# Performance work log

Measured on AMD Instinct MI355X. Metric: run time of the kernel, lower is better.

Reference implementation:

```python
import jax, jax.numpy as jnp
import numpy as np

IMAGE_SIZE = 224
EPS = 1e-8


def _minmax_global(x, eps=EPS):
    # torch normalize_minmax: global min-max over the whole tensor,
    # returning zeros if the range is degenerate.
    lo = x.min()
    hi = x.max()
    y = (x - lo) / (hi - lo + eps)
    return jnp.where(hi - lo < eps, jnp.zeros_like(x), y)


def setup_inputs() -> dict:
    key = jax.random.key(0)
    x = jax.random.normal(key, (16, 1024, 8), dtype=jnp.float32)  # [B, L, D]
    return {"x": x}


def reference(x):
    B, L, D = x.shape
    # --- gramian_angular_field ---
    x_norm = _minmax_global(x) * 2.0 - 1.0                      # [B, L, D]
    theta = jnp.arccos(jnp.clip(x_norm, -1.0 + 1e-6, 1.0 - 1e-6))
    th = jnp.transpose(theta, (0, 2, 1))                        # [B, D, L]
    # fused batched pairwise cos-sum (replaces B*D python-loop kernels)
    cos_sum = jnp.cos(th[:, :, :, None] + th[:, :, None, :])    # [B, D, L, L]
    # per-(b,d) min-max normalization in one pass
    lo = cos_sum.min(axis=(2, 3), keepdims=True)
    hi = cos_sum.max(axis=(2, 3), keepdims=True)
    gaf = jnp.where(hi - lo < EPS,
                    jnp.zeros_like(cos_sum),
                    (cos_sum - lo) / (hi - lo + EPS))
    gaf = gaf.mean(axis=1, keepdims=True)                       # [B, 1, L, L]
    # bilinear resize, align_corners=False (half-pixel centers)
    gaf = jax.image.resize(gaf, (B, 1, IMAGE_SIZE, IMAGE_SIZE),
                           method="linear", antialias=False)
    gaf = jnp.repeat(gaf, 3, axis=1)                            # RGB (grayscale=False)
    # --- final norm(): global shift/scale ---
    out = gaf - gaf.min()
    out = out / (out.max() + 1e-6)
    return out
```

## Files before the change

kernel.cpp:

```cpp
#include <hip/hip_runtime.h>
#include <math.h>

#define B_ 16
#define L_ 1024
#define IMG 224
#define PIX (IMG*IMG)
#define NBD 128

#define OFF_A     0
#define OFF_TERM  128
#define OFF_GPMIN 256
#define OFF_GPMAX 768
#define OFF_T     1280
#define OFF_G     58624

#define CPAD(k) ((((k) >> 4) * 17) + ((k) & 15))

__device__ __forceinline__ float cclip(float xn) {
    return fminf(fmaxf(xn, -1.0f + 1e-6f), 1.0f - 1e-6f);
}
__device__ __forceinline__ int bucketf(float c) {
    int k = (int)((c + 1.0f) * 512.0f);
    return min(1023, max(0, k));
}

template <int NTHR>
__device__ __forceinline__ void block_minmax_share(float mn, float mx, float* red) {
    #pragma unroll
    for (int off = 32; off > 0; off >>= 1) {
        mn = fminf(mn, __shfl_down(mn, off));
        mx = fmaxf(mx, __shfl_down(mx, off));
    }
    const int lane = threadIdx.x & 63;
    const int wave = threadIdx.x >> 6;
    if (lane == 0) { red[2 + wave*2] = mn; red[3 + wave*2] = mx; }
    __syncthreads();
    if (threadIdx.x == 0) {
        #pragma unroll
        for (int w = 1; w < NTHR/64; ++w) {
            mn = fminf(mn, red[2 + w*2]);
            mx = fmaxf(mx, red[3 + w*2]);
        }
        red[0] = mn; red[1] = mx;
    }
    __syncthreads();
}

__global__ __launch_bounds__(1024) void k_bd(const float* __restrict__ x,
                                             float* __restrict__ wsf) {
    __shared__ float red[36];
    __shared__ float corig[L_];
    __shared__ float arr[L_];
    __shared__ int   cnt[1090];
    __shared__ int   pref[1090];
    const int bd = blockIdx.x;
    const int b = bd >> 3, d = bd & 7;
    const int t = threadIdx.x;

    {
        float mn = 1e30f, mx = -1e30f;
        const float4* xv = (const float4*)x;
        #pragma unroll 4
        for (int i = t; i < 32768; i += 1024) {
            float4 v = xv[i];
            mn = fminf(mn, fminf(fminf(v.x, v.y), fminf(v.z, v.w)));
            mx = fmaxf(mx, fmaxf(fmaxf(v.x, v.y), fmaxf(v.z, v.w)));
        }
        block_minmax_share<1024>(mn, mx, red);
    }
    float lo = red[0], hi = red[1], r = hi - lo, sc, sh;
    if (r < 1e-8f) { sc = 0.0f; sh = -1.0f; }
    else           { sc = 2.0f / (r + 1e-8f); sh = -lo*sc - 1.0f; }

    cnt[t] = 0;
    if (t < 66) cnt[1024 + t] = 0;
    float c = cclip(x[((size_t)(b*L_ + t))*8 + d]*sc + sh);
    corig[t] = c;
    block_minmax_share<1024>(c, c, red);
    float cMin = red[0], cMax = red[1];

    atomicAdd(&cnt[CPAD(bucketf(c))], 1);
    __syncthreads();

    if (t < 64) {
        int s = 0;
        #pragma unroll
        for (int e = 0; e < 16; ++e) s += cnt[t*17 + e];
        int v = s;
        #pragma unroll
        for (int o = 1; o < 64; o <<= 1) {
            int u = __shfl_up(v, o);
            if (t >= o) v += u;
        }
        int run = v - s;
        #pragma unroll
        for (int e = 0; e < 16; ++e) { pref[t*17 + e] = run; run += cnt[t*17 + e]; }
        if (t == 63) pref[CPAD(1024)] = run;
    }
    __syncthreads();
    cnt[CPAD(t)] = pref[CPAD(t)];
    __syncthreads();
    {
        int p = atomicAdd(&cnt[CPAD(bucketf(c))], 1);
        arr[p] = c;
    }
    __syncthreads();

    float rowmin = 1e30f;
    {
        float ci = c;
        float si = sqrtf(fmaxf(1.0f - ci*ci, 0.0f));
        int kt = bucketf(-ci);
        int lo_p = pref[CPAD(kt)], hi_p = pref[CPAD(kt + 1)];
        int start = lo_p, end = hi_p;
        if (lo_p > 0)   start = pref[CPAD(bucketf(arr[lo_p - 1]))];
        if (hi_p < L_)  end   = pref[CPAD(bucketf(arr[hi_p]) + 1)];
        for (int p = start; p < end; ++p) {
            float cj = arr[p];
            float sj = sqrtf(fmaxf(1.0f - cj*cj, 0.0f));
            rowmin = fminf(rowmin, ci*cj - si*sj);
        }
    }
    block_minmax_share<1024>(rowmin, -1e30f, red);
    if (t == 0) {
        float plo = red[0];
        float phi = fmaxf(2.0f*cMin*cMin - 1.0f, 2.0f*cMax*cMax - 1.0f);
        float rr  = phi - plo;
        float inv = (rr < 1e-8f) ? 0.0f : 1.0f / (rr + 1e-8f);
        wsf[OFF_A + bd]    = inv * 0.125f;
        wsf[OFF_TERM + bd] = plo * inv * 0.125f;
    }

    if (t < IMG) {
        const float SC = 1024.0f / 224.0f;
        float syf = (t + 0.5f)*SC - 0.5f;
        int i0 = (int)floorf(syf);
        i0 = max(0, min(i0, L_ - 2));
        float f = syf - (float)i0;
        float ca = corig[i0], cb = corig[i0 + 1];
        float sa = sqrtf(fmaxf(1.0f - ca*ca, 0.0f));
        float sb = sqrtf(fmaxf(1.0f - cb*cb, 0.0f));
        size_t base = OFF_T + ((size_t)(b*IMG + t))*16;
        wsf[base + d]     = ca + f*(cb - ca);
        wsf[base + 8 + d] = sa + f*(sb - sa);
    }
}

__global__ __launch_bounds__(256) void k_resize(float* __restrict__ wsf) {
    __shared__ float lds_y[112];
    __shared__ float red[16];
    int b     = blockIdx.x >> 5;
    int strip = blockIdx.x & 31;
    const float* tb = wsf + OFF_T + (size_t)b*IMG*16;
    int t = threadIdx.x;
    if (t < 112) lds_y[t] = tb[strip*112 + t];
    __syncthreads();
    int ox = min(t, IMG-1);
    bool active = (t < IMG);
    const float4* xt = (const float4*)(tb + (size_t)ox*16);
    float4 cx0 = xt[0], cx1 = xt[1], sx0 = xt[2], sx1 = xt[3];
    const float4* av = (const float4*)(wsf + OFF_A + b*8);
    float4 a0 = av[0], a1 = av[1];
    float bias = 0.f;
    #pragma unroll
    for (int dd = 0; dd < 8; ++dd) bias += wsf[OFF_TERM + b*8 + dd];
    float mn = 1e30f, mx = -1e30f;
    #pragma unroll
    for (int rr = 0; rr < 7; ++rr) {
        const float* Y = lds_y + rr*16;
        float acc;
        acc  = (a0.x*Y[0])*cx0.x - (a0.x*Y[ 8])*sx0.x;
        acc += (a0.y*Y[1])*cx0.y - (a0.y*Y[ 9])*sx0.y;
        acc += (a0.z*Y[2])*cx0.z - (a0.z*Y[10])*sx0.z;
        acc += (a0.w*Y[3])*cx0.w - (a0.w*Y[11])*sx0.w;
        acc += (a1.x*Y[4])*cx1.x - (a1.x*Y[12])*sx1.x;
        acc += (a1.y*Y[5])*cx1.y - (a1.y*Y[13])*sx1.y;
        acc += (a1.z*Y[6])*cx1.z - (a1.z*Y[14])*sx1.z;
        acc += (a1.w*Y[7])*cx1.w - (a1.w*Y[15])*sx1.w;
        float g = acc - bias;
        if (active) {
            int oy = strip*7 + rr;
            wsf[OFF_G + ((size_t)(b*IMG + oy))*IMG + ox] = g;
            mn = fminf(mn, g);
            mx = fmaxf(mx, g);
        }
    }
    block_minmax_share<256>(mn, mx, red);
    if (t == 0) {
        wsf[OFF_GPMIN + blockIdx.x] = red[0];
        wsf[OFF_GPMAX + blockIdx.x] = red[1];
    }
}

__global__ __launch_bounds__(256) void k_out(const float* __restrict__ wsf,
                                             float* __restrict__ out) {
    __shared__ float red[16];
    int t = threadIdx.x;
    float pmn = fminf(wsf[OFF_GPMIN + t], wsf[OFF_GPMIN + t + 256]);
    float pmx = fmaxf(wsf[OFF_GPMAX + t], wsf[OFF_GPMAX + t + 256]);
    block_minmax_share<256>(pmn, pmx, red);
    float gmin = red[0];
    float scale = 1.0f / ((red[1] - gmin) + 1e-6f);
    int idx = blockIdx.x*256 + t;
    float4 gv = ((const float4*)(wsf + OFF_G))[idx];
    float4 v;
    v.x = (gv.x - gmin)*scale;
    v.y = (gv.y - gmin)*scale;
    v.z = (gv.z - gmin)*scale;
    v.w = (gv.w - gmin)*scale;
    int b   = idx / (PIX/4);
    int rem = idx - b*(PIX/4);
    float4* ob = (float4*)(out + (size_t)b*3*PIX) + rem;
    ob[0]         = v;
    ob[PIX/4]     = v;
    ob[2*(PIX/4)] = v;
}

extern "C" void kernel_launch(void* const* d_in, const int* in_sizes, int n_in,
                              void* d_out, int out_size, void* d_ws, size_t ws_size,
                              hipStream_t stream) {
    const float* x = (const float*)d_in[0];
    float* out     = (float*)d_out;
    float* wsf     = (float*)d_ws;

    k_bd    <<<NBD,            1024, 0, stream>>>(x, wsf);
    k_resize<<<512,            256,  0, stream>>>(wsf);
    k_out   <<<(B_*PIX/4)/256, 256,  0, stream>>>(wsf, out);
}
```

Before: 28.07 us.

## Fuse resize into k_bd using inter-block flag barrier per batch

Removes the separate resize kernel launch by having the 8 blocks of each batch signal one another through global flag words and spin-wait until all per-d coefficients are written. Each block then computes 28 output rows of the resized image, reusing its pooled LDS, and writes the per-block min/max partials. This saves one kernel launch and its tail, but it relies on all 128 blocks being co-resident and adds spin-wait latency. Only 128 blocks now do the resize work instead of 512.

```diff
diff --git a/kernel.cpp b/kernel.cpp
--- a/kernel.cpp
+++ b/kernel.cpp
@@ -6,13 +6,15 @@
 #define IMG 224
 #define PIX (IMG*IMG)
 #define NBD 128
-
-#define OFF_A     0
-#define OFF_TERM  128
-#define OFF_GPMIN 256
-#define OFF_GPMAX 768
-#define OFF_T     1280
-#define OFF_G     58624
+#define MAGIC 0x1357BEEFu
+
+#define OFF_DONE  0
+#define OFF_A     1024
+#define OFF_TERM  1152
+#define OFF_GPMIN 1280
+#define OFF_GPMAX 1408
+#define OFF_T     1536
+#define OFF_G     58880
 
 #define CPAD(k) ((((k) >> 4) * 17) + ((k) & 15))
 
@@ -47,12 +49,16 @@
 }
 
 __global__ __launch_bounds__(1024) void k_bd(const float* __restrict__ x,
-                                             float* __restrict__ wsf) {
+                                             float* __restrict__ wsf,
+                                             unsigned* __restrict__ wsu) {
     __shared__ float red[36];
-    __shared__ float corig[L_];
-    __shared__ float arr[L_];
-    __shared__ int   cnt[1090];
-    __shared__ int   pref[1090];
+    __shared__ __align__(16) float POOL[4352];
+    float* corig = POOL;
+    float* arr   = POOL + 1024;
+    int*   cnt   = (int*)(POOL + 2048);
+    int*   pref  = ((int*)(POOL + 2048)) + 1090;
+    float* ylds  = POOL;
+
     const int bd = blockIdx.x;
     const int b = bd >> 3, d = bd & 7;
     const int t = threadIdx.x;
@@ -144,51 +150,73 @@
         wsf[base + d]     = ca + f*(cb - ca);
         wsf[base + 8 + d] = sa + f*(sb - sa);
     }
-}
-
-__global__ __launch_bounds__(256) void k_resize(float* __restrict__ wsf) {
-    __shared__ float lds_y[112];
-    __shared__ float red[16];
-    int b     = blockIdx.x >> 5;
-    int strip = blockIdx.x & 31;
-    const float* tb = wsf + OFF_T + (size_t)b*IMG*16;
-    int t = threadIdx.x;
-    if (t < 112) lds_y[t] = tb[strip*112 + t];
-    __syncthreads();
-    int ox = min(t, IMG-1);
-    bool active = (t < IMG);
-    const float4* xt = (const float4*)(tb + (size_t)ox*16);
-    float4 cx0 = xt[0], cx1 = xt[1], sx0 = xt[2], sx1 = xt[3];
-    const float4* av = (const float4*)(wsf + OFF_A + b*8);
-    float4 a0 = av[0], a1 = av[1];
-    float bias = 0.f;
-    #pragma unroll
-    for (int dd = 0; dd < 8; ++dd) bias += wsf[OFF_TERM + b*8 + dd];
-    float mn = 1e30f, mx = -1e30f;
-    #pragma unroll
-    for (int rr = 0; rr < 7; ++rr) {
-        const float* Y = lds_y + rr*16;
-        float acc;
-        acc  = (a0.x*Y[0])*cx0.x - (a0.x*Y[ 8])*sx0.x;
-        acc += (a0.y*Y[1])*cx0.y - (a0.y*Y[ 9])*sx0.y;
-        acc += (a0.z*Y[2])*cx0.z - (a0.z*Y[10])*sx0.z;
-        acc += (a0.w*Y[3])*cx0.w - (a0.w*Y[11])*sx0.w;
-        acc += (a1.x*Y[4])*cx1.x - (a1.x*Y[12])*sx1.x;
-        acc += (a1.y*Y[5])*cx1.y - (a1.y*Y[13])*sx1.y;
-        acc += (a1.z*Y[6])*cx1.z - (a1.z*Y[14])*sx1.z;
-        acc += (a1.w*Y[7])*cx1.w - (a1.w*Y[15])*sx1.w;
-        float g = acc - bias;
-        if (active) {
-            int oy = strip*7 + rr;
-            wsf[OFF_G + ((size_t)(b*IMG + oy))*IMG + ox] = g;
-            mn = fminf(mn, g);
-            mx = fmaxf(mx, g);
-        }
-    }
-    block_minmax_share<256>(mn, mx, red);
+    __syncthreads();
+
     if (t == 0) {
-        wsf[OFF_GPMIN + blockIdx.x] = red[0];
-        wsf[OFF_GPMAX + blockIdx.x] = red[1];
+        __threadfence();
+        #pragma unroll
+        for (int cons = 0; cons < 8; ++cons)
+            if (cons != d)
+                __hip_atomic_store(&wsu[OFF_DONE + b*64 + d*8 + cons], MAGIC,
+                                   __ATOMIC_RELAXED, __HIP_MEMORY_SCOPE_AGENT);
+        for (int p = 0; p < 8; ++p) {
+            if (p == d) continue;
+            while (__hip_atomic_load(&wsu[OFF_DONE + b*64 + p*8 + d],
+                                     __ATOMIC_RELAXED, __HIP_MEMORY_SCOPE_AGENT)
+                   != MAGIC)
+                __builtin_amdgcn_s_sleep(1);
+        }
+        __threadfence();
+        #pragma unroll
+        for (int p = 0; p < 8; ++p)
+            if (p != d)
+                __hip_atomic_store(&wsu[OFF_DONE + b*64 + p*8 + d], 0u,
+                                   __ATOMIC_RELAXED, __HIP_MEMORY_SCOPE_AGENT);
+    }
+    __syncthreads();
+
+    {
+        const int R0 = d*28;
+        const float* tb = wsf + OFF_T + (size_t)b*IMG*16;
+        for (int e = t; e < 448; e += 1024) ylds[e] = tb[(size_t)R0*16 + e];
+        __syncthreads();
+        int tx = t & 255, ty = t >> 8;
+        bool active = (tx < IMG);
+        int ox = min(tx, IMG - 1);
+        const float4* xt = (const float4*)(tb + (size_t)ox*16);
+        float4 cx0 = xt[0], cx1 = xt[1], sx0 = xt[2], sx1 = xt[3];
+        const float4* av = (const float4*)(wsf + OFF_A + b*8);
+        float4 a0 = av[0], a1 = av[1];
+        float bias = 0.f;
+        #pragma unroll
+        for (int dd = 0; dd < 8; ++dd) bias += wsf[OFF_TERM + b*8 + dd];
+        float mn = 1e30f, mx = -1e30f;
+        #pragma unroll
+        for (int rr = 0; rr < 7; ++rr) {
+            int ry = ty*7 + rr;
+            const float* Y = ylds + ry*16;
+            float acc;
+            acc  = (a0.x*Y[0])*cx0.x - (a0.x*Y[ 8])*sx0.x;
+            acc += (a0.y*Y[1])*cx0.y - (a0.y*Y[ 9])*sx0.y;
+            acc += (a0.z*Y[2])*cx0.z - (a0.z*Y[10])*sx0.z;
+            acc += (a0.w*Y[3])*cx0.w - (a0.w*Y[11])*sx0.w;
+            acc += (a1.x*Y[4])*cx1.x - (a1.x*Y[12])*sx1.x;
+            acc += (a1.y*Y[5])*cx1.y - (a1.y*Y[13])*sx1.y;
+            acc += (a1.z*Y[6])*cx1.z - (a1.z*Y[14])*sx1.z;
+            acc += (a1.w*Y[7])*cx1.w - (a1.w*Y[15])*sx1.w;
+            float g = acc - bias;
+            if (active) {
+                int oy = R0 + ry;
+                wsf[OFF_G + (size_t)b*PIX + (size_t)oy*IMG + ox] = g;
+                mn = fminf(mn, g);
+                mx = fmaxf(mx, g);
+            }
+        }
+        block_minmax_share<1024>(mn, mx, red);
+        if (t == 0) {
+            wsf[OFF_GPMIN + bd] = red[0];
+            wsf[OFF_GPMAX + bd] = red[1];
+        }
     }
 }
 
@@ -196,8 +224,8 @@
                                              float* __restrict__ out) {
     __shared__ float red[16];
     int t = threadIdx.x;
-    float pmn = fminf(wsf[OFF_GPMIN + t], wsf[OFF_GPMIN + t + 256]);
-    float pmx = fmaxf(wsf[OFF_GPMAX + t], wsf[OFF_GPMAX + t + 256]);
+    float pmn = (t < 128) ? wsf[OFF_GPMIN + t] :  1e30f;
+    float pmx = (t < 128) ? wsf[OFF_GPMAX + t] : -1e30f;
     block_minmax_share<256>(pmn, pmx, red);
     float gmin = red[0];
     float scale = 1.0f / ((red[1] - gmin) + 1e-6f);
@@ -222,8 +250,8 @@
     const float* x = (const float*)d_in[0];
     float* out     = (float*)d_out;
     float* wsf     = (float*)d_ws;
-
-    k_bd    <<<NBD,            1024, 0, stream>>>(x, wsf);
-    k_resize<<<512,            256,  0, stream>>>(wsf);
-    k_out   <<<(B_*PIX/4)/256, 256,  0, stream>>>(wsf, out);
-}
+    unsigned* wsu  = (unsigned*)d_ws;
+
+    k_bd <<<NBD,            1024, 0, stream>>>(x, wsf, wsu);
+    k_out<<<(B_*PIX/4)/256, 256,  0, stream>>>(wsf, out);
+}
```

New measurement: 35.86 us. +27.7%, slower.

## Fuse resize and output kernels with an atomic-counter grid barrier

Applied to the files above, without the earlier changes.

Merges the resize kernel and the final normalisation/output kernel into a single launch. Consumer blocks spin on a global atomic counter that each resize block increments with release semantics, and the counter is reset by the first kernel. This is meant to remove one kernel launch boundary and its drain/fill gap. In exchange it depends on the resize blocks being scheduled before or alongside the spinning consumer blocks (784 of them), which risks deadlock or wasted CU time while they poll.

```diff
diff --git a/kernel.cpp b/kernel.cpp
--- a/kernel.cpp
+++ b/kernel.cpp
@@ -6,13 +6,15 @@
 #define IMG 224
 #define PIX (IMG*IMG)
 #define NBD 128
+#define NRES 512
 
 #define OFF_A     0
 #define OFF_TERM  128
 #define OFF_GPMIN 256
 #define OFF_GPMAX 768
-#define OFF_T     1280
-#define OFF_G     58624
+#define OFF_CTR   1280
+#define OFF_T     1284
+#define OFF_G     58628
 
 #define CPAD(k) ((((k) >> 4) * 17) + ((k) & 15))
 
@@ -47,7 +49,8 @@
 }
 
 __global__ __launch_bounds__(1024) void k_bd(const float* __restrict__ x,
-                                             float* __restrict__ wsf) {
+                                             float* __restrict__ wsf,
+                                             unsigned* __restrict__ wsu) {
     __shared__ float red[36];
     __shared__ float corig[L_];
     __shared__ float arr[L_];
@@ -56,6 +59,8 @@
     const int bd = blockIdx.x;
     const int b = bd >> 3, d = bd & 7;
     const int t = threadIdx.x;
+
+    if (bd == 0 && t == 0) wsu[OFF_CTR] = 0u;
 
     {
         float mn = 1e30f, mx = -1e30f;
@@ -146,74 +151,84 @@
     }
 }
 
-__global__ __launch_bounds__(256) void k_resize(float* __restrict__ wsf) {
-    __shared__ float lds_y[112];
+__global__ __launch_bounds__(256) void k_fused(float* __restrict__ wsf,
+                                               unsigned* __restrict__ wsu,
+                                               float* __restrict__ out) {
     __shared__ float red[16];
-    int b     = blockIdx.x >> 5;
-    int strip = blockIdx.x & 31;
-    const float* tb = wsf + OFF_T + (size_t)b*IMG*16;
-    int t = threadIdx.x;
-    if (t < 112) lds_y[t] = tb[strip*112 + t];
-    __syncthreads();
-    int ox = min(t, IMG-1);
-    bool active = (t < IMG);
-    const float4* xt = (const float4*)(tb + (size_t)ox*16);
-    float4 cx0 = xt[0], cx1 = xt[1], sx0 = xt[2], sx1 = xt[3];
-    const float4* av = (const float4*)(wsf + OFF_A + b*8);
-    float4 a0 = av[0], a1 = av[1];
-    float bias = 0.f;
-    #pragma unroll
-    for (int dd = 0; dd < 8; ++dd) bias += wsf[OFF_TERM + b*8 + dd];
-    float mn = 1e30f, mx = -1e30f;
-    #pragma unroll
-    for (int rr = 0; rr < 7; ++rr) {
-        const float* Y = lds_y + rr*16;
-        float acc;
-        acc  = (a0.x*Y[0])*cx0.x - (a0.x*Y[ 8])*sx0.x;
-        acc += (a0.y*Y[1])*cx0.y - (a0.y*Y[ 9])*sx0.y;
-        acc += (a0.z*Y[2])*cx0.z - (a0.z*Y[10])*sx0.z;
-        acc += (a0.w*Y[3])*cx0.w - (a0.w*Y[11])*sx0.w;
-        acc += (a1.x*Y[4])*cx1.x - (a1.x*Y[12])*sx1.x;
-        acc += (a1.y*Y[5])*cx1.y - (a1.y*Y[13])*sx1.y;
-        acc += (a1.z*Y[6])*cx1.z - (a1.z*Y[14])*sx1.z;
-        acc += (a1.w*Y[7])*cx1.w - (a1.w*Y[15])*sx1.w;
-        float g = acc - bias;
-        if (active) {
-            int oy = strip*7 + rr;
-            wsf[OFF_G + ((size_t)(b*IMG + oy))*IMG + ox] = g;
-            mn = fminf(mn, g);
-            mx = fmaxf(mx, g);
-        }
-    }
-    block_minmax_share<256>(mn, mx, red);
-    if (t == 0) {
-        wsf[OFF_GPMIN + blockIdx.x] = red[0];
-        wsf[OFF_GPMAX + blockIdx.x] = red[1];
-    }
-}
-
-__global__ __launch_bounds__(256) void k_out(const float* __restrict__ wsf,
-                                             float* __restrict__ out) {
-    __shared__ float red[16];
-    int t = threadIdx.x;
-    float pmn = fminf(wsf[OFF_GPMIN + t], wsf[OFF_GPMIN + t + 256]);
-    float pmx = fmaxf(wsf[OFF_GPMAX + t], wsf[OFF_GPMAX + t + 256]);
-    block_minmax_share<256>(pmn, pmx, red);
-    float gmin = red[0];
-    float scale = 1.0f / ((red[1] - gmin) + 1e-6f);
-    int idx = blockIdx.x*256 + t;
-    float4 gv = ((const float4*)(wsf + OFF_G))[idx];
-    float4 v;
-    v.x = (gv.x - gmin)*scale;
-    v.y = (gv.y - gmin)*scale;
-    v.z = (gv.z - gmin)*scale;
-    v.w = (gv.w - gmin)*scale;
-    int b   = idx / (PIX/4);
-    int rem = idx - b*(PIX/4);
-    float4* ob = (float4*)(out + (size_t)b*3*PIX) + rem;
-    ob[0]         = v;
-    ob[PIX/4]     = v;
-    ob[2*(PIX/4)] = v;
+    const int t = threadIdx.x;
+
+    if (blockIdx.x < NRES) {
+        __shared__ float lds_y[112];
+        int b     = blockIdx.x >> 5;
+        int strip = blockIdx.x & 31;
+        const float* tb = wsf + OFF_T + (size_t)b*IMG*16;
+        if (t < 112) lds_y[t] = tb[strip*112 + t];
+        __syncthreads();
+        int ox = min(t, IMG-1);
+        bool active = (t < IMG);
+        const float4* xt = (const float4*)(tb + (size_t)ox*16);
+        float4 cx0 = xt[0], cx1 = xt[1], sx0 = xt[2], sx1 = xt[3];
+        const float4* av = (const float4*)(wsf + OFF_A + b*8);
+        float4 a0 = av[0], a1 = av[1];
+        float bias = 0.f;
+        #pragma unroll
+        for (int dd = 0; dd < 8; ++dd) bias += wsf[OFF_TERM + b*8 + dd];
+        float mn = 1e30f, mx = -1e30f;
+        #pragma unroll
+        for (int rr = 0; rr < 7; ++rr) {
+            const float* Y = lds_y + rr*16;
+            float acc;
+            acc  = (a0.x*Y[0])*cx0.x - (a0.x*Y[ 8])*sx0.x;
+            acc += (a0.y*Y[1])*cx0.y - (a0.y*Y[ 9])*sx0.y;
+            acc += (a0.z*Y[2])*cx0.z - (a0.z*Y[10])*sx0.z;
+            acc += (a0.w*Y[3])*cx0.w - (a0.w*Y[11])*sx0.w;
+            acc += (a1.x*Y[4])*cx1.x - (a1.x*Y[12])*sx1.x;
+            acc += (a1.y*Y[5])*cx1.y - (a1.y*Y[13])*sx1.y;
+            acc += (a1.z*Y[6])*cx1.z - (a1.z*Y[14])*sx1.z;
+            acc += (a1.w*Y[7])*cx1.w - (a1.w*Y[15])*sx1.w;
+            float g = acc - bias;
+            if (active) {
+                int oy = strip*7 + rr;
+                wsf[OFF_G + ((size_t)(b*IMG + oy))*IMG + ox] = g;
+                mn = fminf(mn, g);
+                mx = fmaxf(mx, g);
+            }
+        }
+        block_minmax_share<256>(mn, mx, red);
+        if (t == 0) {
+            wsf[OFF_GPMIN + blockIdx.x] = red[0];
+            wsf[OFF_GPMAX + blockIdx.x] = red[1];
+            __hip_atomic_fetch_add(&wsu[OFF_CTR], 1u,
+                                   __ATOMIC_RELEASE, __HIP_MEMORY_SCOPE_AGENT);
+        }
+    } else {
+        if (t == 0) {
+            while (__hip_atomic_load(&wsu[OFF_CTR], __ATOMIC_RELAXED,
+                                     __HIP_MEMORY_SCOPE_AGENT) < (unsigned)NRES)
+                __builtin_amdgcn_s_sleep(2);
+            (void)__hip_atomic_load(&wsu[OFF_CTR], __ATOMIC_ACQUIRE,
+                                    __HIP_MEMORY_SCOPE_AGENT);
+        }
+        __syncthreads();
+        float pmn = fminf(wsf[OFF_GPMIN + t], wsf[OFF_GPMIN + t + 256]);
+        float pmx = fmaxf(wsf[OFF_GPMAX + t], wsf[OFF_GPMAX + t + 256]);
+        block_minmax_share<256>(pmn, pmx, red);
+        float gmin = red[0];
+        float scale = 1.0f / ((red[1] - gmin) + 1e-6f);
+        int idx = (blockIdx.x - NRES)*256 + t;
+        float4 gv = ((const float4*)(wsf + OFF_G))[idx];
+        float4 v;
+        v.x = (gv.x - gmin)*scale;
+        v.y = (gv.y - gmin)*scale;
+        v.z = (gv.z - gmin)*scale;
+        v.w = (gv.w - gmin)*scale;
+        int b   = idx / (PIX/4);
+        int rem = idx - b*(PIX/4);
+        float4* ob = (float4*)(out + (size_t)b*3*PIX) + rem;
+        ob[0]         = v;
+        ob[PIX/4]     = v;
+        ob[2*(PIX/4)] = v;
+    }
 }
 
 extern "C" void kernel_launch(void* const* d_in, const int* in_sizes, int n_in,
@@ -222,8 +237,8 @@
     const float* x = (const float*)d_in[0];
     float* out     = (float*)d_out;
     float* wsf     = (float*)d_ws;
-
-    k_bd    <<<NBD,            1024, 0, stream>>>(x, wsf);
-    k_resize<<<512,            256,  0, stream>>>(wsf);
-    k_out   <<<(B_*PIX/4)/256, 256,  0, stream>>>(wsf, out);
-}
+    unsigned* wsu  = (unsigned*)d_ws;
+
+    k_bd   <<<NBD,                    1024, 0, stream>>>(x, wsf, wsu);
+    k_fused<<<NRES + (B_*PIX/4)/256,  256,  0, stream>>>(wsf, wsu, out);
+}
```

New measurement: 62.26 us. 122% more time.
